# Kernel tuning notes

Measured on AMD Instinct MI355X. Metric: run time of the kernel, lower is better.

Reference implementation:

```python
import jax, jax.numpy as jnp
import numpy as np

N_CLUSTERS = 8
ENC_IN = 862
SEQ_LEN = 720
PRED_LEN = 336
BATCH = 64


def setup_inputs() -> dict:
    key = jax.random.key(0)
    k1, k2, k3, k4 = jax.random.split(key, 4)
    x = jax.random.normal(k1, (BATCH, ENC_IN, SEQ_LEN), dtype=jnp.float32)
    clusters = jax.random.randint(k2, (ENC_IN,), 0, N_CLUSTERS, dtype=jnp.int64)
    # Per-cluster Linear(seq_len -> pred_len): weight [P, S], bias [P], like nn.Linear
    bound = 1.0 / np.sqrt(SEQ_LEN)
    W = jax.random.uniform(k3, (N_CLUSTERS, PRED_LEN, SEQ_LEN), dtype=jnp.float32, minval=-bound, maxval=bound)
    b = jax.random.uniform(k4, (N_CLUSTERS, PRED_LEN), dtype=jnp.float32, minval=-bound, maxval=bound)
    return {"x": x, "clusters": clusters, "W": W, "b": b}


def reference(x, clusters, W, b):
    # Gather each channel's cluster weight/bias, then batched per-channel GEMV.
    Wc = W[clusters]            # [C, P, S]
    bc = b[clusters]            # [C, P]
    # out[b, c, p] = sum_s x[b, c, s] * Wc[c, p, s] + bc[c, p]
    out = jnp.einsum('bcs,cps->bcp', x, Wc) + bc[None, :, :]
    return out
```

## Files before the change

### kernel.cpp

```cpp
#include <hip/hip_runtime.h>
#include <stdint.h>

#define N_CL    8
#define C_IN    862
#define SEQ     720
#define SEQP    768
#define PRED    336
#define BATCH   64
#define BK      64
#define NCH     (SEQP / BK)
#define NT      (PRED / 16)
#define XBSTRIDE ((size_t)C_IN * SEQ)

typedef __attribute__((ext_vector_type(8))) __bf16 bf16x8;
typedef __attribute__((ext_vector_type(4))) float  floatx4;

__device__ __forceinline__ void async16(const void* g, void* l) {
  __builtin_amdgcn_global_load_lds(
      (__attribute__((address_space(1))) unsigned int*)(uintptr_t)g,
      (__attribute__((address_space(3))) unsigned int*)l,
      16, 0, 0);
}

__global__ void wconv_kernel(const float* __restrict__ W, __bf16* __restrict__ Wb) {
  const int row = blockIdx.x;
  const float* src = W + (size_t)row * SEQ;
  __bf16* dst = Wb + (size_t)row * SEQP;
  for (int s = threadIdx.x; s < SEQP; s += blockDim.x) {
    float v = (s < SEQ) ? src[s] : 0.0f;
    dst[s] = (__bf16)v;
  }
}

#define A_BYTES 16384
#define B_BYTES 43008

__global__ __launch_bounds__(256, 2) void clin_kernel(
    const float* __restrict__ x, const int* __restrict__ clusters,
    const __bf16* __restrict__ Wb, const float* __restrict__ bias,
    float* __restrict__ out) {
  __shared__ __attribute__((aligned(128))) unsigned char smem[A_BYTES + B_BYTES];
  unsigned char* As = smem;
  unsigned char* Bs = smem + A_BYTES;

  const int c    = blockIdx.x;
  const int cl   = clusters[c];
  const int tid  = threadIdx.x;
  const int wave = tid >> 6;
  const int lane = tid & 63;
  const int q    = lane >> 4;
  const int ln   = lane & 15;

  const float*  xc = x  + (size_t)c * SEQ;
  const __bf16* wc = Wb + (size_t)cl * PRED * SEQP;

  floatx4 acc[NT];
#pragma unroll
  for (int t = 0; t < NT; ++t) acc[t] = (floatx4){0.f, 0.f, 0.f, 0.f};

  const int bA_r  = lane >> 4;
  const int bA_pg = lane & 15;
  const int bB_r  = lane >> 3;
  const int bB_pg = lane & 7;

  for (int chunk = 0; chunk < NCH; ++chunk) {
    const int k0 = chunk * BK;

    for (int i = wave; i < 42; i += 4) {
      int r  = (i << 3) + bB_r;
      int lg = bB_pg ^ (r & 7);
      async16(wc + (size_t)r * SEQP + k0 + (lg << 3), Bs + i * 1024);
    }

    if (k0 + BK <= SEQ) {
      for (int i = wave; i < 16; i += 4) {
        int r  = (i << 2) + bA_r;
        int lg = bA_pg ^ (r & 15);
        async16(xc + (size_t)r * XBSTRIDE + k0 + (lg << 2), As + i * 1024);
      }
    } else {
      for (int i = wave; i < 16; i += 4) {
        int r  = (i << 2) + bA_r;
        int lg = bA_pg ^ (r & 15);
        int s  = k0 + (lg << 2);
        floatx4 v = (floatx4){0.f, 0.f, 0.f, 0.f};
        if (s < SEQ) v = *(const floatx4*)(xc + (size_t)r * XBSTRIDE + s);
        *(floatx4*)(As + r * 256 + (bA_pg << 4)) = v;
      }
    }
    __syncthreads();

    const int mrow = (wave << 4) + ln;
#pragma unroll
    for (int kk = 0; kk < BK; kk += 32) {
      int lg0 = (kk >> 2) + (q << 1);
      floatx4 af0 = *(const floatx4*)(As + mrow * 256 + (((lg0    ) ^ ln) << 4));
      floatx4 af1 = *(const floatx4*)(As + mrow * 256 + (((lg0 + 1) ^ ln) << 4));
      bf16x8 a;
      a[0] = (__bf16)af0[0]; a[1] = (__bf16)af0[1];
      a[2] = (__bf16)af0[2]; a[3] = (__bf16)af0[3];
      a[4] = (__bf16)af1[0]; a[5] = (__bf16)af1[1];
      a[6] = (__bf16)af1[2]; a[7] = (__bf16)af1[3];

      int lgB  = (kk >> 3) + q;
      int nsw  = ln & 7;
#pragma unroll
      for (int t = 0; t < NT; ++t) {
        int n = (t << 4) + ln;
        bf16x8 b = *(const bf16x8*)(Bs + n * 128 + ((lgB ^ nsw) << 4));
        acc[t] = __builtin_amdgcn_mfma_f32_16x16x32_bf16(a, b, acc[t], 0, 0, 0);
      }
    }
    __syncthreads();
  }

  const float* bc = bias + cl * PRED;
#pragma unroll
  for (int t = 0; t < NT; ++t) {
    int p = (t << 4) + ln;
    float bv = bc[p];
#pragma unroll
    for (int r = 0; r < 4; ++r) {
      int brow = (wave << 4) + (q << 2) + r;
      out[((size_t)brow * C_IN + c) * PRED + p] = acc[t][r] + bv;
    }
  }
}

extern "C" void kernel_launch(void* const* d_in, const int* in_sizes, int n_in,
                              void* d_out, int out_size, void* d_ws, size_t ws_size,
                              hipStream_t stream) {
  const float* x   = (const float*)d_in[0];
  const int*   cls = (const int*)d_in[1];
  const float* W   = (const float*)d_in[2];
  const float* b   = (const float*)d_in[3];
  float* out = (float*)d_out;
  __bf16* Wb = (__bf16*)d_ws;

  hipLaunchKernelGGL(wconv_kernel, dim3(N_CL * PRED), dim3(256), 0, stream, W, Wb);
  hipLaunchKernelGGL(clin_kernel, dim3(C_IN), dim3(256), 0, stream,
                     x, cls, Wb, b, out);
}
```

Baseline: 275.3 us.

## Split waves over N tiles, stage x as bf16 in LDS

Each wave now covers all 64 batch rows and a slice of 5 output column tiles, with wave 3 taking the leftover 21st tile. Before, each wave covered 16 batch rows across all 21 column tiles. The x chunk is loaded synchronously, converted to bf16 once and stored in a swizzled bf16 layout, which halves A's LDS footprint and removes the per-wave fp32-to-bf16 conversion. The launch bound rises to 3 blocks per CU. The goal is to cut the number of B fragment reads from LDS and the redundant conversion work. In exchange, the async load of x is dropped and wave 3 carries extra load.

```diff
diff --git a/kernel.cpp b/kernel.cpp
--- a/kernel.cpp
+++ b/kernel.cpp
@@ -9,7 +9,6 @@
 #define BATCH   64
 #define BK      64
 #define NCH     (SEQP / BK)
-#define NT      (PRED / 16)
 #define XBSTRIDE ((size_t)C_IN * SEQ)
 
 typedef __attribute__((ext_vector_type(8))) __bf16 bf16x8;
@@ -32,10 +31,10 @@
   }
 }
 
-#define A_BYTES 16384
+#define A_BYTES 8192
 #define B_BYTES 43008
 
-__global__ __launch_bounds__(256, 2) void clin_kernel(
+__global__ __launch_bounds__(256, 3) void clin_kernel(
     const float* __restrict__ x, const int* __restrict__ clusters,
     const __bf16* __restrict__ Wb, const float* __restrict__ bias,
     float* __restrict__ out) {
@@ -50,18 +49,31 @@
   const int lane = tid & 63;
   const int q    = lane >> 4;
   const int ln   = lane & 15;
+  const int m7   = ln & 7;
 
   const float*  xc = x  + (size_t)c * SEQ;
   const __bf16* wc = Wb + (size_t)cl * PRED * SEQP;
 
-  floatx4 acc[NT];
+  floatx4 acc[4][5];
+  floatx4 accx[4];
 #pragma unroll
-  for (int t = 0; t < NT; ++t) acc[t] = (floatx4){0.f, 0.f, 0.f, 0.f};
+  for (int mt = 0; mt < 4; ++mt) {
+#pragma unroll
+    for (int t = 0; t < 5; ++t) acc[mt][t] = (floatx4){0.f, 0.f, 0.f, 0.f};
+    accx[mt] = (floatx4){0.f, 0.f, 0.f, 0.f};
+  }
 
-  const int bA_r  = lane >> 4;
-  const int bA_pg = lane & 15;
+  const int ar  = tid >> 2;
+  const int ag0 = (tid & 3) << 1;
+  const int am  = ar & 7;
+  const uint32_t aoff0 = (uint32_t)ar * 128 + (((ag0    ) ^ am) << 4);
+  const uint32_t aoff1 = (uint32_t)ar * 128 + (((ag0 + 1) ^ am) << 4);
+  const float* asrc = xc + (size_t)ar * XBSTRIDE;
+
   const int bB_r  = lane >> 3;
   const int bB_pg = lane & 7;
+
+  const int nb = wave * 5;
 
   for (int chunk = 0; chunk < NCH; ++chunk) {
     const int k0 = chunk * BK;
@@ -73,42 +85,58 @@
     }
 
     if (k0 + BK <= SEQ) {
-      for (int i = wave; i < 16; i += 4) {
-        int r  = (i << 2) + bA_r;
-        int lg = bA_pg ^ (r & 15);
-        async16(xc + (size_t)r * XBSTRIDE + k0 + (lg << 2), As + i * 1024);
+      const float* s = asrc + k0 + (ag0 << 3);
+      floatx4 f0 = *(const floatx4*)(s);
+      floatx4 f1 = *(const floatx4*)(s + 4);
+      floatx4 f2 = *(const floatx4*)(s + 8);
+      floatx4 f3 = *(const floatx4*)(s + 12);
+      bf16x8 h0, h1;
+      h0[0] = (__bf16)f0[0]; h0[1] = (__bf16)f0[1];
+      h0[2] = (__bf16)f0[2]; h0[3] = (__bf16)f0[3];
+      h0[4] = (__bf16)f1[0]; h0[5] = (__bf16)f1[1];
+      h0[6] = (__bf16)f1[2]; h0[7] = (__bf16)f1[3];
+      h1[0] = (__bf16)f2[0]; h1[1] = (__bf16)f2[1];
+      h1[2] = (__bf16)f2[2]; h1[3] = (__bf16)f2[3];
+      h1[4] = (__bf16)f3[0]; h1[5] = (__bf16)f3[1];
+      h1[6] = (__bf16)f3[2]; h1[7] = (__bf16)f3[3];
+      *(bf16x8*)(As + aoff0) = h0;
+      *(bf16x8*)(As + aoff1) = h1;
+    } else {
+      float tmp[16];
+#pragma unroll
+      for (int j = 0; j < 16; ++j) {
+        int k = k0 + (ag0 << 3) + j;
+        tmp[j] = (k < SEQ) ? asrc[k] : 0.0f;
       }
-    } else {
-      for (int i = wave; i < 16; i += 4) {
-        int r  = (i << 2) + bA_r;
-        int lg = bA_pg ^ (r & 15);
-        int s  = k0 + (lg << 2);
-        floatx4 v = (floatx4){0.f, 0.f, 0.f, 0.f};
-        if (s < SEQ) v = *(const floatx4*)(xc + (size_t)r * XBSTRIDE + s);
-        *(floatx4*)(As + r * 256 + (bA_pg << 4)) = v;
-      }
+      bf16x8 h0, h1;
+#pragma unroll
+      for (int j = 0; j < 8; ++j) { h0[j] = (__bf16)tmp[j]; h1[j] = (__bf16)tmp[8 + j]; }
+      *(bf16x8*)(As + aoff0) = h0;
+      *(bf16x8*)(As + aoff1) = h1;
     }
     __syncthreads();
 
-    const int mrow = (wave << 4) + ln;
 #pragma unroll
     for (int kk = 0; kk < BK; kk += 32) {
-      int lg0 = (kk >> 2) + (q << 1);
-      floatx4 af0 = *(const floatx4*)(As + mrow * 256 + (((lg0    ) ^ ln) << 4));
-      floatx4 af1 = *(const floatx4*)(As + mrow * 256 + (((lg0 + 1) ^ ln) << 4));
-      bf16x8 a;
-      a[0] = (__bf16)af0[0]; a[1] = (__bf16)af0[1];
-      a[2] = (__bf16)af0[2]; a[3] = (__bf16)af0[3];
-      a[4] = (__bf16)af1[0]; a[5] = (__bf16)af1[1];
-      a[6] = (__bf16)af1[2]; a[7] = (__bf16)af1[3];
-
-      int lgB  = (kk >> 3) + q;
-      int nsw  = ln & 7;
+      const int gA = (kk >> 3) + q;
+      bf16x8 a[4];
 #pragma unroll
-      for (int t = 0; t < NT; ++t) {
-        int n = (t << 4) + ln;
-        bf16x8 b = *(const bf16x8*)(Bs + n * 128 + ((lgB ^ nsw) << 4));
-        acc[t] = __builtin_amdgcn_mfma_f32_16x16x32_bf16(a, b, acc[t], 0, 0, 0);
+      for (int mt = 0; mt < 4; ++mt)
+        a[mt] = *(const bf16x8*)(As + ((mt << 4) + ln) * 128 + ((gA ^ m7) << 4));
+#pragma unroll
+      for (int t = 0; t < 5; ++t) {
+        int n = ((nb + t) << 4) + ln;
+        bf16x8 b = *(const bf16x8*)(Bs + n * 128 + ((gA ^ m7) << 4));
+#pragma unroll
+        for (int mt = 0; mt < 4; ++mt)
+          acc[mt][t] = __builtin_amdgcn_mfma_f32_16x16x32_bf16(a[mt], b, acc[mt][t], 0, 0, 0);
+      }
+      if (wave == 3) {
+        int n = (20 << 4) + ln;
+        bf16x8 b = *(const bf16x8*)(Bs + n * 128 + ((gA ^ m7) << 4));
+#pragma unroll
+        for (int mt = 0; mt < 4; ++mt)
+          accx[mt] = __builtin_amdgcn_mfma_f32_16x16x32_bf16(a[mt], b, accx[mt], 0, 0, 0);
       }
     }
     __syncthreads();
@@ -116,13 +144,28 @@
 
   const float* bc = bias + cl * PRED;
 #pragma unroll
-  for (int t = 0; t < NT; ++t) {
-    int p = (t << 4) + ln;
+  for (int t = 0; t < 5; ++t) {
+    int p = ((nb + t) << 4) + ln;
     float bv = bc[p];
 #pragma unroll
-    for (int r = 0; r < 4; ++r) {
-      int brow = (wave << 4) + (q << 2) + r;
-      out[((size_t)brow * C_IN + c) * PRED + p] = acc[t][r] + bv;
+    for (int mt = 0; mt < 4; ++mt) {
+#pragma unroll
+      for (int r = 0; r < 4; ++r) {
+        int brow = (mt << 4) + (q << 2) + r;
+        out[((size_t)brow * C_IN + c) * PRED + p] = acc[mt][t][r] + bv;
+      }
+    }
+  }
+  if (wave == 3) {
+    int p = (20 << 4) + ln;
+    float bv = bc[p];
+#pragma unroll
+    for (int mt = 0; mt < 4; ++mt) {
+#pragma unroll
+      for (int r = 0; r < 4; ++r) {
+        int brow = (mt << 4) + (q << 2) + r;
+        out[((size_t)brow * C_IN + c) * PRED + p] = accx[mt][r] + bv;
+      }
     }
   }
 }
```

After: 307.8 us. +11.8%, slower.

## Pair same-cluster channels per block with 32x32 MFMA and register-prefetched x

Applied to the files above, without the earlier changes.

A new prep kernel groups channels by cluster on the device. Each GEMM block then handles two channels of the same cluster, so the bf16 weight tile loaded into LDS is reused for 128 rows instead of 64, roughly halving weight traffic per output. The block grows to 512 threads and switches to 32x32x16 MFMAs. x is converted to bf16 before it is stored in LDS, and the next chunk of x is prefetched into registers while the current chunk computes. The cost is an extra single-block prep launch with an O(C^2) rank loop, and ragged clusters leave idle half-blocks.

```diff
diff --git a/kernel.cpp b/kernel.cpp
--- a/kernel.cpp
+++ b/kernel.cpp
@@ -6,20 +6,50 @@
 #define SEQ     720
 #define SEQP    768
 #define PRED    336
-#define BATCH   64
 #define BK      64
-#define NCH     (SEQP / BK)
-#define NT      (PRED / 16)
-#define XBSTRIDE ((size_t)C_IN * SEQ)
-
-typedef __attribute__((ext_vector_type(8))) __bf16 bf16x8;
-typedef __attribute__((ext_vector_type(4))) float  floatx4;
+#define NCH     12
+#define MBLOCKS 435
+
+#define WB_BYTES 4128768
+
+typedef __attribute__((ext_vector_type(8)))  __bf16 bf16x8;
+typedef __attribute__((ext_vector_type(4)))  float  floatx4;
+typedef __attribute__((ext_vector_type(16))) float  floatx16;
 
 __device__ __forceinline__ void async16(const void* g, void* l) {
   __builtin_amdgcn_global_load_lds(
       (__attribute__((address_space(1))) unsigned int*)(uintptr_t)g,
       (__attribute__((address_space(3))) unsigned int*)l,
       16, 0, 0);
+}
+
+__global__ void prep_kernel(const int* __restrict__ clusters, int* __restrict__ meta) {
+  __shared__ int cls_s[C_IN];
+  __shared__ int cnt[N_CL];
+  __shared__ int cst[N_CL + 1], bst[N_CL + 1];
+  const int t = threadIdx.x;
+  if (t < N_CL) cnt[t] = 0;
+  __syncthreads();
+  int cl = -1;
+  if (t < C_IN) { cl = clusters[t]; cls_s[t] = cl; }
+  __syncthreads();
+  int rank = 0;
+  if (t < C_IN) {
+    for (int j = 0; j < t; ++j) rank += (cls_s[j] == cl) ? 1 : 0;
+    atomicAdd(&cnt[cl], 1);
+  }
+  __syncthreads();
+  if (t == 0) {
+    int a = 0, b = 0;
+    for (int g = 0; g < N_CL; ++g) {
+      cst[g] = a; bst[g] = b;
+      a += cnt[g]; b += (cnt[g] + 1) >> 1;
+    }
+    cst[N_CL] = a; bst[N_CL] = b;
+  }
+  __syncthreads();
+  if (t < C_IN) meta[cst[cl] + rank] = t;
+  if (t < N_CL + 1) { meta[C_IN + t] = cst[t]; meta[C_IN + 9 + t] = bst[t]; }
 }
 
 __global__ void wconv_kernel(const float* __restrict__ W, __bf16* __restrict__ Wb) {
@@ -35,94 +65,153 @@
 #define A_BYTES 16384
 #define B_BYTES 43008
 
-__global__ __launch_bounds__(256, 2) void clin_kernel(
-    const float* __restrict__ x, const int* __restrict__ clusters,
+__global__ __launch_bounds__(512, 2) void clin_kernel(
+    const float* __restrict__ x, const int* __restrict__ meta,
     const __bf16* __restrict__ Wb, const float* __restrict__ bias,
     float* __restrict__ out) {
   __shared__ __attribute__((aligned(128))) unsigned char smem[A_BYTES + B_BYTES];
   unsigned char* As = smem;
   unsigned char* Bs = smem + A_BYTES;
 
-  const int c    = blockIdx.x;
-  const int cl   = clusters[c];
-  const int tid  = threadIdx.x;
-  const int wave = tid >> 6;
-  const int lane = tid & 63;
-  const int q    = lane >> 4;
-  const int ln   = lane & 15;
-
-  const float*  xc = x  + (size_t)c * SEQ;
-  const __bf16* wc = Wb + (size_t)cl * PRED * SEQP;
-
-  floatx4 acc[NT];
-#pragma unroll
-  for (int t = 0; t < NT; ++t) acc[t] = (floatx4){0.f, 0.f, 0.f, 0.f};
-
-  const int bA_r  = lane >> 4;
-  const int bA_pg = lane & 15;
-  const int bB_r  = lane >> 3;
-  const int bB_pg = lane & 7;
-
-  for (int chunk = 0; chunk < NCH; ++chunk) {
-    const int k0 = chunk * BK;
-
-    for (int i = wave; i < 42; i += 4) {
-      int r  = (i << 3) + bB_r;
-      int lg = bB_pg ^ (r & 7);
-      async16(wc + (size_t)r * SEQP + k0 + (lg << 3), Bs + i * 1024);
-    }
-
-    if (k0 + BK <= SEQ) {
-      for (int i = wave; i < 16; i += 4) {
-        int r  = (i << 2) + bA_r;
-        int lg = bA_pg ^ (r & 15);
-        async16(xc + (size_t)r * XBSTRIDE + k0 + (lg << 2), As + i * 1024);
-      }
-    } else {
-      for (int i = wave; i < 16; i += 4) {
-        int r  = (i << 2) + bA_r;
-        int lg = bA_pg ^ (r & 15);
-        int s  = k0 + (lg << 2);
-        floatx4 v = (floatx4){0.f, 0.f, 0.f, 0.f};
-        if (s < SEQ) v = *(const floatx4*)(xc + (size_t)r * XBSTRIDE + s);
-        *(floatx4*)(As + r * 256 + (bA_pg << 4)) = v;
-      }
-    }
+  const int* cstart = meta + C_IN;
+  const int* bstart = meta + C_IN + 9;
+  const int bid = blockIdx.x;
+  if (bid >= bstart[N_CL]) return;
+
+  int g = 0;
+#pragma unroll
+  for (int i = 1; i < N_CL; ++i) g = (bid >= bstart[i]) ? i : g;
+  const int lb     = bid - bstart[g];
+  const int nch_g  = cstart[g + 1] - cstart[g];
+  const int ch0    = meta[cstart[g] + (lb << 1)];
+  const bool v1    = ((lb << 1) + 1) < nch_g;
+  const int ch1    = v1 ? meta[cstart[g] + (lb << 1) + 1] : ch0;
+
+  const int t    = threadIdx.x;
+  const int wave = t >> 6;
+  const int lane = t & 63;
+  const int col  = lane & 31;
+  const int half = lane >> 5;
+  const int nt0  = wave >> 1;
+  const int mt0  = (wave & 1) << 1;
+
+  const __bf16* wc = Wb + (size_t)g * PRED * SEQP;
+
+  floatx16 acc[2][3];
+#pragma unroll
+  for (int mi = 0; mi < 2; ++mi)
+#pragma unroll
+    for (int s = 0; s < 3; ++s)
+#pragma unroll
+      for (int r = 0; r < 16; ++r) acc[mi][s][r] = 0.0f;
+
+  const int rt    = t >> 2;
+  const int batch = rt & 63;
+  const int chA   = (rt >> 6) ? ch1 : ch0;
+  const float* srcp = x + ((size_t)batch * C_IN + chA) * SEQ;
+  const int koff  = (t & 3) << 4;
+  const int bg0   = (t & 3) << 1;
+  const uint32_t aw0 = (uint32_t)rt * 128 + (((bg0    ) ^ (rt & 7)) << 4);
+  const uint32_t aw1 = (uint32_t)rt * 128 + (((bg0 + 1) ^ (rt & 7)) << 4);
+
+  floatx4 f0, f1, f2, f3;
+  {
+    const float* s = srcp + koff;
+    f0 = *(const floatx4*)(s);     f1 = *(const floatx4*)(s + 4);
+    f2 = *(const floatx4*)(s + 8); f3 = *(const floatx4*)(s + 12);
+    bf16x8 h0, h1;
+#pragma unroll
+    for (int j = 0; j < 4; ++j) {
+      h0[j] = (__bf16)f0[j]; h0[4 + j] = (__bf16)f1[j];
+      h1[j] = (__bf16)f2[j]; h1[4 + j] = (__bf16)f3[j];
+    }
+    *(bf16x8*)(As + aw0) = h0;
+    *(bf16x8*)(As + aw1) = h1;
+    for (int i = wave; i < 42; i += 8) {
+      int r  = (i << 3) + (lane >> 3);
+      int lg = (lane & 7) ^ (r & 7);
+      async16(wc + (size_t)r * SEQP + (lg << 3), Bs + i * 1024);
+    }
+  }
+
+  for (int k = 0; k < NCH; ++k) {
     __syncthreads();
 
-    const int mrow = (wave << 4) + ln;
-#pragma unroll
-    for (int kk = 0; kk < BK; kk += 32) {
-      int lg0 = (kk >> 2) + (q << 1);
-      floatx4 af0 = *(const floatx4*)(As + mrow * 256 + (((lg0    ) ^ ln) << 4));
-      floatx4 af1 = *(const floatx4*)(As + mrow * 256 + (((lg0 + 1) ^ ln) << 4));
-      bf16x8 a;
-      a[0] = (__bf16)af0[0]; a[1] = (__bf16)af0[1];
-      a[2] = (__bf16)af0[2]; a[3] = (__bf16)af0[3];
-      a[4] = (__bf16)af1[0]; a[5] = (__bf16)af1[1];
-      a[6] = (__bf16)af1[2]; a[7] = (__bf16)af1[3];
-
-      int lgB  = (kk >> 3) + q;
-      int nsw  = ln & 7;
-#pragma unroll
-      for (int t = 0; t < NT; ++t) {
-        int n = (t << 4) + ln;
-        bf16x8 b = *(const bf16x8*)(Bs + n * 128 + ((lgB ^ nsw) << 4));
-        acc[t] = __builtin_amdgcn_mfma_f32_16x16x32_bf16(a, b, acc[t], 0, 0, 0);
-      }
-    }
+    const bool have_next = (k + 1 < NCH);
+    if (have_next) {
+      const int kb = (k + 1) * BK + koff;
+      if (kb + 16 <= SEQ) {
+        const float* s = srcp + kb;
+        f0 = *(const floatx4*)(s);     f1 = *(const floatx4*)(s + 4);
+        f2 = *(const floatx4*)(s + 8); f3 = *(const floatx4*)(s + 12);
+      } else {
+        f0 = (floatx4){0.f,0.f,0.f,0.f}; f1 = f0; f2 = f0; f3 = f0;
+      }
+    }
+
+#pragma unroll
+    for (int ks = 0; ks < 4; ++ks) {
+      const int g2 = (ks << 1) + half;
+      const int r0 = (mt0 << 5) + col;
+      const int r1 = r0 + 32;
+      bf16x8 a0 = *(const bf16x8*)(As + r0 * 128 + ((g2 ^ (r0 & 7)) << 4));
+      bf16x8 a1 = *(const bf16x8*)(As + r1 * 128 + ((g2 ^ (r1 & 7)) << 4));
+#pragma unroll
+      for (int s = 0; s < 3; ++s) {
+        const int tl = nt0 + (s << 2);
+        if (tl <= 10) {
+          const int cc = (tl == 10) ? (col & 15) : col;
+          const int rb = (tl << 5) + cc;
+          bf16x8 b = *(const bf16x8*)(Bs + rb * 128 + ((g2 ^ (rb & 7)) << 4));
+          acc[0][s] = __builtin_amdgcn_mfma_f32_32x32x16_bf16(a0, b, acc[0][s], 0, 0, 0);
+          acc[1][s] = __builtin_amdgcn_mfma_f32_32x32x16_bf16(a1, b, acc[1][s], 0, 0, 0);
+        }
+      }
+    }
+
     __syncthreads();
-  }
-
-  const float* bc = bias + cl * PRED;
-#pragma unroll
-  for (int t = 0; t < NT; ++t) {
-    int p = (t << 4) + ln;
-    float bv = bc[p];
-#pragma unroll
-    for (int r = 0; r < 4; ++r) {
-      int brow = (wave << 4) + (q << 2) + r;
-      out[((size_t)brow * C_IN + c) * PRED + p] = acc[t][r] + bv;
+
+    if (have_next) {
+      const int k0b = (k + 1) * BK;
+      for (int i = wave; i < 42; i += 8) {
+        int r  = (i << 3) + (lane >> 3);
+        int lg = (lane & 7) ^ (r & 7);
+        async16(wc + (size_t)r * SEQP + k0b + (lg << 3), Bs + i * 1024);
+      }
+      bf16x8 h0, h1;
+#pragma unroll
+      for (int j = 0; j < 4; ++j) {
+        h0[j] = (__bf16)f0[j]; h0[4 + j] = (__bf16)f1[j];
+        h1[j] = (__bf16)f2[j]; h1[4 + j] = (__bf16)f3[j];
+      }
+      *(bf16x8*)(As + aw0) = h0;
+      *(bf16x8*)(As + aw1) = h1;
+    }
+  }
+
+  const bool cvalid = (wave & 1) ? v1 : true;
+  const int  chO    = (wave & 1) ? ch1 : ch0;
+  if (cvalid) {
+    const float* bc = bias + g * PRED;
+#pragma unroll
+    for (int s = 0; s < 3; ++s) {
+      const int tl = nt0 + (s << 2);
+      if (tl <= 10) {
+        const int p = (tl << 5) + col;
+        if (p < PRED) {
+          const float bv = bc[p];
+#pragma unroll
+          for (int mi = 0; mi < 2; ++mi) {
+            const int mt = mt0 + mi;
+#pragma unroll
+            for (int r = 0; r < 16; ++r) {
+              const int m  = (r & 3) + ((r >> 2) << 3) + (half << 2);
+              const int bb = ((mt << 5) + m) & 63;
+              out[((size_t)bb * C_IN + chO) * PRED + p] = acc[mi][s][r] + bv;
+            }
+          }
+        }
+      }
     }
   }
 }
@@ -136,8 +225,10 @@
   const float* b   = (const float*)d_in[3];
   float* out = (float*)d_out;
   __bf16* Wb = (__bf16*)d_ws;
-
-  hipLaunchKernelGGL(wconv_kernel, dim3(N_CL * PRED), dim3(256), 0, stream, W, Wb);
-  hipLaunchKernelGGL(clin_kernel, dim3(C_IN), dim3(256), 0, stream,
-                     x, cls, Wb, b, out);
-}
+  int* meta  = (int*)((unsigned char*)d_ws + WB_BYTES);
+
+  hipLaunchKernelGGL(prep_kernel,  dim3(1),            dim3(1024), 0, stream, cls, meta);
+  hipLaunchKernelGGL(wconv_kernel, dim3(N_CL * PRED),  dim3(256),  0, stream, W, Wb);
+  hipLaunchKernelGGL(clin_kernel,  dim3(MBLOCKS),      dim3(512),  0, stream,
+                     x, meta, Wb, b, out);
+}
```

Result: slower. 292.2 us (+6.1%).
